# Kernel tuning notes

Hardware: AMD Instinct MI355X
Metric: run time of the kernel (lower is better)

Reference implementation:

```python
import jax, jax.numpy as jnp
import numpy as np

NA, NPA, NT = 4096, 8192, 4096  # authors, papers, terms
HEADS = 8

def _ln(x, g, b):
    m = jnp.mean(x, -1, keepdims=True)
    v = jnp.var(x, -1, keepdims=True)
    return (x - m) * jax.lax.rsqrt(v + 1e-5) * g + b

def _gat(x_src, x_dst, src, dst, W, a_s, a_d, b, n_dst):
    # PyG-style GATConv (shared lin for src/dst, no self loops), per edge type.
    heads, outc = a_s.shape
    h_s = (x_src @ W).reshape(-1, heads, outc)
    h_d = (x_dst @ W).reshape(-1, heads, outc)
    e = jax.nn.leaky_relu(jnp.sum(h_s * a_s, -1)[src] + jnp.sum(h_d * a_d, -1)[dst], 0.2)  # [E,H]
    m = jax.ops.segment_max(e, dst, num_segments=n_dst)
    m = jnp.where(jnp.isfinite(m), m, 0.0)
    w = jnp.exp(e - m[dst])
    den = jax.ops.segment_sum(w, dst, num_segments=n_dst)
    alpha = w / (den[dst] + 1e-16)
    out = jax.ops.segment_sum(h_s[src] * alpha[..., None], dst, num_segments=n_dst)
    return out.reshape(n_dst, heads * outc) + b

def _gtl(x, peQ, peK, db, Wq, bq, Wk, bk, Wv, bv, Wo, bo, g1, be1, Wf1, bf1, Wf2, bf2, g2, be2):
    # PE-modulated dense multi-head attention + FFN, pre/post LN residual blocks.
    N, D = x.shape
    dh = D // HEADS
    Q = (x @ Wq + bq + peQ).reshape(N, HEADS, dh)
    K = (x @ Wk + bk + peK).reshape(N, HEADS, dh)
    V = (x @ Wv + bv).reshape(N, HEADS, dh)
    s = jnp.einsum('nhd,mhd->hnm', Q, K) / jnp.sqrt(jnp.float32(dh)) + db[None, None, :]
    o = jnp.einsum('hnm,mhd->nhd', jax.nn.softmax(s, -1), V).reshape(N, D) @ Wo + bo
    x = _ln(x + o, g1, be1)
    f = jax.nn.relu(x @ Wf1 + bf1) @ Wf2 + bf2
    return _ln(x + f, g2, be2)

def _forward(F, I):
    (x_author, x_paper, x_term, original_A, t1_W, t1_b, t2_W, t2_b, t3_W, t3_b,
     gat1_W, gat1_as, gat1_ad, gat1_b, gat2_W, gat2_as, gat2_ad, gat2_b,
     pe_embed, peWQ, peWK,
     gt_Wq, gt_bq, gt_Wk, gt_bk, gt_Wv, gt_bv, gt_Wo, gt_bo,
     gt_g1, gt_be1, gt_Wf1, gt_bf1, gt_Wf2, gt_bf2, gt_g2, gt_be2,
     cat_W, cat_b, mlp_W1, mlp_b1, mlp_W2, mlp_b2) = F
    (ap_src, ap_dst, pa_src, pa_dst, pt_src, pt_dst, tp_src, tp_dst, deg) = I
    xa = jax.nn.relu(x_author @ t1_W + t1_b)
    xp = jax.nn.relu(x_paper @ t2_W + t2_b)
    xt = jax.nn.relu(x_term @ t3_W + t3_b)
    # to_hetero GAT layer 1 (heads=8, out=128): sum over incoming edge types, relu
    h_p1 = jax.nn.relu(_gat(xa, xp, ap_src, ap_dst, gat1_W[0], gat1_as[0], gat1_ad[0], gat1_b[0], NPA)
                       + _gat(xt, xp, tp_src, tp_dst, gat1_W[3], gat1_as[3], gat1_ad[3], gat1_b[3], NPA))
    h_a1 = jax.nn.relu(_gat(xp, xa, pa_src, pa_dst, gat1_W[1], gat1_as[1], gat1_ad[1], gat1_b[1], NA))
    # layer 2 (heads=1); only author output feeds the graph transformer
    h_a2 = _gat(h_p1, h_a1, pa_src, pa_dst, gat2_W[1], gat2_as[1], gat2_ad[1], gat2_b[1], NA)
    # learned positional encodings + adjacency reconstruction loss
    peQ = pe_embed @ peWQ
    peK = pe_embed @ peWK
    S = jax.nn.sigmoid(peQ @ peK.T)  # [NA, NA]
    loss_pe = jnp.mean((S[None] - original_A) ** 2)
    db = jnp.log(jnp.maximum(deg.astype(jnp.float32), 1.0))  # degree key bias
    x = h_a2
    outs = [x]
    for i in range(gt_Wq.shape[0]):
        x = _gtl(x, peQ, peK, db, gt_Wq[i], gt_bq[i], gt_Wk[i], gt_bk[i], gt_Wv[i], gt_bv[i],
                 gt_Wo[i], gt_bo[i], gt_g1[i], gt_be1[i], gt_Wf1[i], gt_bf1[i], gt_Wf2[i], gt_bf2[i],
                 gt_g2[i], gt_be2[i])
        outs.append(x)
    x_gt = jax.nn.relu(jnp.concatenate(outs, -1) @ cat_W + cat_b)
    logits = jax.nn.relu(x_gt @ mlp_W1 + mlp_b1) @ mlp_W2 + mlp_b2
    return loss_pe, jax.nn.softmax(logits, -1), x_gt

def setup_inputs() -> dict:
    key = jax.random.key(0)
    ks = iter(jax.random.split(key, 100))
    def rn(sh, s=1.0):
        return jax.random.normal(next(ks), sh, jnp.float32) * s
    def ri(sh, hi, lo=0):
        return jax.random.randint(next(ks), sh, lo, hi)
    d = {}
    d['x_author'] = rn((NA, 334)); d['x_paper'] = rn((NPA, 512)); d['x_term'] = rn((NT, 128))
    d['ap_src'] = ri((80000,), NA); d['ap_dst'] = ri((80000,), NPA)
    d['pa_src'] = ri((80000,), NPA); d['pa_dst'] = ri((80000,), NA)
    d['pt_src'] = ri((160000,), NPA); d['pt_dst'] = ri((160000,), NT)
    d['tp_src'] = ri((160000,), NT); d['tp_dst'] = ri((160000,), NPA)
    d['original_A'] = (jax.random.uniform(next(ks), (4, NA, NA)) < 0.005).astype(jnp.float32)
    d['deg'] = ri((NA,), 64, 1)
    p = 0.05
    d['t1_W'] = rn((334, 128), p); d['t1_b'] = jnp.zeros((128,))
    d['t2_W'] = rn((512, 128), p); d['t2_b'] = jnp.zeros((128,))
    d['t3_W'] = rn((128, 128), p); d['t3_b'] = jnp.zeros((128,))
    d['gat1_W'] = rn((4, 128, 1024), p); d['gat1_as'] = rn((4, 8, 128), p)
    d['gat1_ad'] = rn((4, 8, 128), p); d['gat1_b'] = jnp.zeros((4, 1024))
    d['gat2_W'] = rn((4, 1024, 128), p); d['gat2_as'] = rn((4, 1, 128), p)
    d['gat2_ad'] = rn((4, 1, 128), p); d['gat2_b'] = jnp.zeros((4, 128))
    d['pe_embed'] = rn((NA, 128), p); d['peWQ'] = rn((128, 128), p); d['peWK'] = rn((128, 128), p)
    d['gt_Wq'] = rn((2, 128, 128), p); d['gt_bq'] = jnp.zeros((2, 128))
    d['gt_Wk'] = rn((2, 128, 128), p); d['gt_bk'] = jnp.zeros((2, 128))
    d['gt_Wv'] = rn((2, 128, 128), p); d['gt_bv'] = jnp.zeros((2, 128))
    d['gt_Wo'] = rn((2, 128, 128), p); d['gt_bo'] = jnp.zeros((2, 128))
    d['gt_g1'] = jnp.ones((2, 128)); d['gt_be1'] = jnp.zeros((2, 128))
    d['gt_Wf1'] = rn((2, 128, 256), p); d['gt_bf1'] = jnp.zeros((2, 256))
    d['gt_Wf2'] = rn((2, 256, 128), p); d['gt_bf2'] = jnp.zeros((2, 128))
    d['gt_g2'] = jnp.ones((2, 128)); d['gt_be2'] = jnp.zeros((2, 128))
    d['cat_W'] = rn((384, 128), p); d['cat_b'] = jnp.zeros((128,))
    d['mlp_W1'] = rn((128, 256), p); d['mlp_b1'] = jnp.zeros((256,))
    d['mlp_W2'] = rn((256, 4), p); d['mlp_b2'] = jnp.zeros((4,))
    return d

def reference(x_author, x_paper, x_term, ap_src, ap_dst, pa_src, pa_dst, pt_src, pt_dst, tp_src, tp_dst, original_A, deg, t1_W, t1_b, t2_W, t2_b, t3_W, t3_b, gat1_W, gat1_as, gat1_ad, gat1_b, gat2_W, gat2_as, gat2_ad, gat2_b, pe_embed, peWQ, peWK, gt_Wq, gt_bq, gt_Wk, gt_bk, gt_Wv, gt_bv, gt_Wo, gt_bo, gt_g1, gt_be1, gt_Wf1, gt_bf1, gt_Wf2, gt_bf2, gt_g2, gt_be2, cat_W, cat_b, mlp_W1, mlp_b1, mlp_W2, mlp_b2):
    F = (x_author, x_paper, x_term, original_A, t1_W, t1_b, t2_W, t2_b, t3_W, t3_b,
         gat1_W, gat1_as, gat1_ad, gat1_b, gat2_W, gat2_as, gat2_ad, gat2_b,
         pe_embed, peWQ, peWK,
         gt_Wq, gt_bq, gt_Wk, gt_bk, gt_Wv, gt_bv, gt_Wo, gt_bo,
         gt_g1, gt_be1, gt_Wf1, gt_bf1, gt_Wf2, gt_bf2, gt_g2, gt_be2,
         cat_W, cat_b, mlp_W1, mlp_b1, mlp_W2, mlp_b2)
    I = (ap_src, ap_dst, pa_src, pa_dst, pt_src, pt_dst, tp_src, tp_dst, deg)
    return _forward(F, I)
```

## Files before the change

kernel.cpp:

```cpp
#include <hip/hip_runtime.h>
#include <math.h>

#define NA   4096
#define NPA  8192
#define NT   4096
#define E_AP 80000
#define E_PA 80000
#define E_TP 160000
#define E_TOT (E_AP + E_TP + E_PA)
#define NSLOT (NPA + NPA + NA)
#define ASPLIT 4

typedef __attribute__((ext_vector_type(4))) float f32x4;
typedef __attribute__((ext_vector_type(8))) short s16x8;
typedef __attribute__((ext_vector_type(8))) unsigned short u16x8;
typedef unsigned short ushort_t;

__device__ __forceinline__ ushort_t f2bf(float f){
  unsigned u = __float_as_uint(f);
  unsigned r = u + 0x7fffu + ((u >> 16) & 1u);
  return (ushort_t)(r >> 16);
}
__device__ __forceinline__ float bf2f(ushort_t u){
  return __uint_as_float(((unsigned)u) << 16);
}

template<int ACT, int TN>
__global__ __launch_bounds__(256) void gemm_mfma_k(
    const void* __restrict__ Ain, const void* __restrict__ A2in, const void* __restrict__ A3in,
    int aBf16,
    const float* __restrict__ B, void* __restrict__ Cout, int cBf16,
    const float* __restrict__ bias,
    const float* __restrict__ addmat, int addCols, int addLd,
    const float* __restrict__ lng, const float* __restrict__ lnb,
    float* __restrict__ rdOut,
    int M, int N, int K, int lda, int ldb, int ldc)
{
  const char* A  = (const char*)Ain;
  const char* A2 = (const char*)A2in;
  const char* A3 = (const char*)A3in;
  char* C = (char*)Cout;

  __shared__ __align__(16) ushort_t As[64][40];
  __shared__ __align__(16) ushort_t Bs[TN][40];
  constexpr int NJ = TN / 32;
  int bm = blockIdx.x * 64, bn = blockIdx.y * TN;
  int tid = threadIdx.x;
  int w = tid >> 6, lane = tid & 63, lg = lane >> 4, lid = lane & 15;
  int wm = (w & 1) * 32, wn = (w >> 1) * (TN / 2);
  f32x4 acc[2][NJ];
#pragma unroll
  for (int i = 0; i < 2; ++i)
#pragma unroll
    for (int j = 0; j < NJ; ++j) acc[i][j] = (f32x4){0.f, 0.f, 0.f, 0.f};

  for (int k0 = 0; k0 < K; k0 += 32) {
    {
      int r = tid >> 2, ks = (tid & 3) * 8;
      int kcol = k0 + ks;
      const char* Ab = A;
      if (A2) { int seg = kcol >> 7; Ab = (seg == 0) ? A : ((seg == 1) ? A2 : A3); kcol &= 127; }
      u16x8 v;
      if (aBf16) {
        v = *(const u16x8*)((const ushort_t*)Ab + (size_t)(bm + r) * lda + kcol);
      } else {
        const float* ap = (const float*)Ab + (size_t)(bm + r) * lda + kcol;
#pragma unroll
        for (int j = 0; j < 8; ++j) {
          int gk = k0 + ks + j;
          float fv = (gk < K) ? ap[j] : 0.f;
          v[j] = f2bf(fv);
        }
      }
      *(u16x8*)&As[r][ks] = v;
    }
    if (TN == 128) {
      int n = tid >> 1, ks = (tid & 1) * 16;
      ushort_t tmp[16];
#pragma unroll
      for (int j = 0; j < 16; ++j) {
        int gk = k0 + ks + j;
        float fv = (gk < K) ? B[(size_t)gk * ldb + bn + n] : 0.f;
        tmp[j] = f2bf(fv);
      }
      u16x8 v0, v1;
#pragma unroll
      for (int j = 0; j < 8; ++j) { v0[j] = tmp[j]; v1[j] = tmp[8 + j]; }
      *(u16x8*)&Bs[n][ks] = v0;
      *(u16x8*)&Bs[n][ks + 8] = v1;
    } else {
      int n = tid >> 2, ks = (tid & 3) * 8;
      u16x8 v;
#pragma unroll
      for (int j = 0; j < 8; ++j) {
        int gk = k0 + ks + j;
        float fv = (gk < K) ? B[(size_t)gk * ldb + bn + n] : 0.f;
        v[j] = f2bf(fv);
      }
      *(u16x8*)&Bs[n][ks] = v;
    }
    __syncthreads();
    s16x8 a_frag[2], b_frag[NJ];
#pragma unroll
    for (int i = 0; i < 2; ++i) a_frag[i] = *(s16x8*)&As[wm + i * 16 + lid][lg * 8];
#pragma unroll
    for (int j = 0; j < NJ; ++j) b_frag[j] = *(s16x8*)&Bs[wn + j * 16 + lid][lg * 8];
#pragma unroll
    for (int i = 0; i < 2; ++i)
#pragma unroll
      for (int j = 0; j < NJ; ++j)
        acc[i][j] = __builtin_amdgcn_mfma_f32_16x16x32_bf16(a_frag[i], b_frag[j], acc[i][j], 0, 0, 0);
    __syncthreads();
  }
  if constexpr (ACT == 3) {
    __shared__ float Ct[64][132];
#pragma unroll
    for (int i = 0; i < 2; ++i) {
#pragma unroll
      for (int j = 0; j < NJ; ++j) {
        int coll = wn + j * 16 + lid;
#pragma unroll
        for (int rr = 0; rr < 4; ++rr) {
          int rowl = wm + i * 16 + lg * 4 + rr;
          Ct[rowl][coll] = acc[i][j][rr];
        }
      }
    }
    __syncthreads();
    int row = tid >> 2, part = tid & 3;
    const float* vsel = (bm + row < 8192) ? lng : lnb;
    float rd = 0.f;
    ushort_t* Cu = (ushort_t*)C;
#pragma unroll
    for (int c2 = 0; c2 < 32; ++c2) {
      int c = part * 32 + c2;
      float f = Ct[row][c];
      rd = fmaf(f, vsel[c], rd);
      Cu[(size_t)(bm + row) * ldc + c] = f2bf(f);
    }
    rd += __shfl_xor(rd, 1);
    rd += __shfl_xor(rd, 2);
    if (part == 0) rdOut[bm + row] = rd;
  } else {
#pragma unroll
    for (int i = 0; i < 2; ++i) {
#pragma unroll
      for (int j = 0; j < NJ; ++j) {
        int c = bn + wn + j * 16 + lid;
#pragma unroll
        for (int rr = 0; rr < 4; ++rr) {
          int r = bm + wm + i * 16 + lg * 4 + rr;
          float v = acc[i][j][rr];
          if (bias)   v += bias[c];
          if (addmat && c < addCols) v += addmat[(size_t)r * addLd + c];
          if (ACT == 1) v = fmaxf(v, 0.f);
          if (cBf16) ((ushort_t*)C)[(size_t)r * ldc + c] = f2bf(v);
          else       ((float*)C)[(size_t)r * ldc + c] = v;
        }
      }
    }
  }
}

struct GDesc {
  const void* A; const void* A2;
  const float* B; void* C;
  const float* bias;
  int aBf16, cBf16, act;
  int M, N, K, lda, ldb, ldc;
  int nz, aOffZ, bOffZ, cOffZ;
  int tileStart;
};
struct GDescArr { GDesc d[4]; int nd; };

__global__ __launch_bounds__(256) void gemm_multi_k(GDescArr da){
  int t = blockIdx.x;
  int di = 0;
#pragma unroll
  for (int i = 1; i < 4; ++i) if (i < da.nd && t >= da.d[i].tileStart) di = i;
  const int aBf16 = da.d[di].aBf16, cBf16 = da.d[di].cBf16, act = da.d[di].act;
  const int M = da.d[di].M, N = da.d[di].N, K = da.d[di].K;
  const int lda = da.d[di].lda, ldb = da.d[di].ldb, ldc = da.d[di].ldc;
  int local = t - da.d[di].tileStart;
  int tM = M >> 6;
  int perZ = tM * (N >> 6);
  int z = local / perZ, rem = local - z * perZ;
  int bm = (rem % tM) * 64, bn = (rem / tM) * 64;
  int asz = aBf16 ? 2 : 4;
  const char* A  = (const char*)da.d[di].A  + (size_t)z * da.d[di].aOffZ * asz;
  const char* A2 = da.d[di].A2 ? (const char*)da.d[di].A2 + (size_t)z * da.d[di].aOffZ * asz : nullptr;
  const float* B = da.d[di].B + (size_t)z * da.d[di].bOffZ;
  char* C = (char*)da.d[di].C + (size_t)z * da.d[di].cOffZ * (cBf16 ? 2 : 4);
  const float* bias = da.d[di].bias ? da.d[di].bias + (size_t)z * da.d[di].cOffZ : nullptr;

  __shared__ __align__(16) ushort_t As[64][40];
  __shared__ __align__(16) ushort_t Bs[64][40];
  int tid = threadIdx.x;
  int w = tid >> 6, lane = tid & 63, lg = lane >> 4, lid = lane & 15;
  int wm = (w & 1) * 32, wn = (w >> 1) * 32;
  f32x4 acc[2][2];
#pragma unroll
  for (int i = 0; i < 2; ++i)
#pragma unroll
    for (int j = 0; j < 2; ++j) acc[i][j] = (f32x4){0.f, 0.f, 0.f, 0.f};

  for (int k0 = 0; k0 < K; k0 += 32) {
    {
      int r = tid >> 2, ks = (tid & 3) * 8;
      int kcol = k0 + ks;
      const char* Ab = A;
      if (A2) { int seg = kcol >> 7; Ab = seg ? A2 : A; kcol &= 127; }
      u16x8 v;
      if (aBf16) {
        v = *(const u16x8*)((const ushort_t*)Ab + (size_t)(bm + r) * lda + kcol);
      } else {
        const float* ap = (const float*)Ab + (size_t)(bm + r) * lda + kcol;
#pragma unroll
        for (int j = 0; j < 8; ++j) {
          int gk = k0 + ks + j;
          float fv = (gk < K) ? ap[j] : 0.f;
          v[j] = f2bf(fv);
        }
      }
      *(u16x8*)&As[r][ks] = v;
    }
    {
      int n = tid >> 2, ks = (tid & 3) * 8;
      u16x8 v;
#pragma unroll
      for (int j = 0; j < 8; ++j) {
        int gk = k0 + ks + j;
        float fv = (gk < K) ? B[(size_t)gk * ldb + bn + n] : 0.f;
        v[j] = f2bf(fv);
      }
      *(u16x8*)&Bs[n][ks] = v;
    }
    __syncthreads();
    s16x8 a_frag[2], b_frag[2];
#pragma unroll
    for (int i = 0; i < 2; ++i) a_frag[i] = *(s16x8*)&As[wm + i * 16 + lid][lg * 8];
#pragma unroll
    for (int j = 0; j < 2; ++j) b_frag[j] = *(s16x8*)&Bs[wn + j * 16 + lid][lg * 8];
#pragma unroll
    for (int i = 0; i < 2; ++i)
#pragma unroll
      for (int j = 0; j < 2; ++j)
        acc[i][j] = __builtin_amdgcn_mfma_f32_16x16x32_bf16(a_frag[i], b_frag[j], acc[i][j], 0, 0, 0);
    __syncthreads();
  }
#pragma unroll
  for (int i = 0; i < 2; ++i) {
#pragma unroll
    for (int j = 0; j < 2; ++j) {
      int c = bn + wn + j * 16 + lid;
#pragma unroll
      for (int rr = 0; rr < 4; ++rr) {
        int r = bm + wm + i * 16 + lg * 4 + rr;
        float v = acc[i][j][rr];
        if (bias) v += bias[c];
        if (act == 1) v = fmaxf(v, 0.f);
        if (cBf16) ((ushort_t*)C)[(size_t)r * ldc + c] = f2bf(v);
        else       ((float*)C)[(size_t)r * ldc + c] = v;
      }
    }
  }
}

__global__ void prep_k(const float* __restrict__ gat1_b, const float* __restrict__ gat1_W,
                       const float* __restrict__ Wq, const float* __restrict__ bq,
                       const float* __restrict__ Wk, const float* __restrict__ bk,
                       const float* __restrict__ Wv, const float* __restrict__ bv,
                       const float* __restrict__ peWQ, const float* __restrict__ peWK,
                       const int* __restrict__ deg,
                       const float* __restrict__ gat1_as, const float* __restrict__ gat1_ad,
                       const int* __restrict__ ap_dst, const int* __restrict__ tp_dst,
                       const int* __restrict__ pa_dst,
                       const float* __restrict__ gt_Wo, const float* __restrict__ gt_Wf1,
                       const float* __restrict__ gt_Wf2, const float* __restrict__ cat_W,
                       const float* __restrict__ mlp_W1,
                       float* __restrict__ bsum, float* __restrict__ Wqkv,
                       float* __restrict__ bqkv, float* __restrict__ peW,
                       float* __restrict__ Bstack, float* __restrict__ dbv,
                       float* __restrict__ Ps, float* __restrict__ Pd,
                       int* __restrict__ cnt,
                       ushort_t* __restrict__ Wot, ushort_t* __restrict__ Wf1t,
                       ushort_t* __restrict__ Wf2t, ushort_t* __restrict__ catt,
                       ushort_t* __restrict__ mlp1t, ushort_t* __restrict__ Wqkvt)
{
  int idx = blockIdx.x * blockDim.x + threadIdx.x;
  if (idx < 1024) { bsum[idx] = gat1_b[idx] + gat1_b[3 * 1024 + idx]; return; }
  idx -= 1024;
  if (idx < 2 * 128 * 384) {
    int l = idx / 49152, rem = idx % 49152;
    int k = rem / 384, c = rem % 384;
    float v;
    if (c < 128)      v = Wq[(size_t)l * 16384 + k * 128 + c];
    else if (c < 256) v = Wk[(size_t)l * 16384 + k * 128 + c - 128];
    else              v = Wv[(size_t)l * 16384 + k * 128 + c - 256];
    Wqkv[(size_t)l * 49152 + k * 384 + c] = v;
    return;
  }
  idx -= 2 * 128 * 384;
  if (idx < 2 * 384) {
    int l = idx / 384, c = idx % 384;
    float v;
    if (c < 128)      v = bq[l * 128 + c];
    else if (c < 256) v = bk[l * 128 + c - 128];
    else              v = bv[l * 128 + c - 256];
    bqkv[l * 384 + c] = v;
    return;
  }
  idx -= 2 * 384;
  if (idx < 128 * 256) {
    int k = idx / 256, c = idx % 256;
    peW[k * 256 + c] = (c < 128) ? peWQ[k * 128 + c] : peWK[k * 128 + c - 128];
    return;
  }
  idx -= 128 * 256;
  if (idx < 256 * 1024) {
    int k = idx / 1024, c = idx % 1024;
    Bstack[idx] = (k < 128) ? gat1_W[(size_t)k * 1024 + c]
                            : gat1_W[(size_t)3 * 131072 + (size_t)(k - 128) * 1024 + c];
    return;
  }
  idx -= 256 * 1024;
  if (idx < NA) { dbv[idx] = logf(fmaxf((float)deg[idx], 1.f)); return; }
  idx -= NA;
  if (idx < 3 * 1024) {
    const int wsel[3] = {0, 3, 1};
    int type = idx / 1024, rem = idx % 1024;
    int k = rem >> 3, h = rem & 7;
    const float* wr = gat1_W + (size_t)wsel[type] * 131072 + (size_t)k * 1024 + h * 128;
    const float* a1 = gat1_as + wsel[type] * 1024 + h * 128;
    const float* a2 = gat1_ad + wsel[type] * 1024 + h * 128;
    float s1 = 0.f, s2 = 0.f;
    for (int c = 0; c < 128; ++c){ float wv = wr[c]; s1 = fmaf(wv, a1[c], s1); s2 = fmaf(wv, a2[c], s2); }
    Ps[(size_t)type * 1024 + k * 8 + h] = s1;
    Pd[(size_t)type * 1024 + k * 8 + h] = s2;
    return;
  }
  idx -= 3 * 1024;
  if (idx < E_TOT) {
    int slot;
    if (idx < E_AP)             slot = ap_dst[idx];
    else if (idx < E_AP + E_TP) slot = NPA + tp_dst[idx - E_AP];
    else                        slot = 2 * NPA + pa_dst[idx - E_AP - E_TP];
    atomicAdd(&cnt[slot], 1);
    return;
  }
  idx -= E_TOT;
  if (idx < 2 * 128 * 128) {
    int l = idx / 16384, rem = idx % 16384;
    int n = rem / 128, k = rem % 128;
    Wot[idx] = f2bf(gt_Wo[(size_t)l * 16384 + k * 128 + n]);
    return;
  }
  idx -= 2 * 128 * 128;
  if (idx < 2 * 256 * 128) {
    int l = idx / 32768, rem = idx % 32768;
    int n = rem / 128, k = rem % 128;
    Wf1t[idx] = f2bf(gt_Wf1[(size_t)l * 32768 + k * 256 + n]);
    return;
  }
  idx -= 2 * 256 * 128;
  if (idx < 2 * 128 * 256) {
    int l = idx / 32768, rem = idx % 32768;
    int n = rem / 256, k = rem % 256;
    Wf2t[idx] = f2bf(gt_Wf2[(size_t)l * 32768 + k * 128 + n]);
    return;
  }
  idx -= 2 * 128 * 256;
  if (idx < 128 * 384) {
    int n = idx / 384, k = idx % 384;
    catt[idx] = f2bf(cat_W[(size_t)k * 128 + n]);
    return;
  }
  idx -= 128 * 384;
  if (idx < 256 * 128) {
    int n = idx / 128, k = idx % 128;
    mlp1t[idx] = f2bf(mlp_W1[(size_t)k * 256 + n]);
    return;
  }
  idx -= 256 * 128;
  if (idx < 2 * 384 * 128) {
    int l = idx / 49152, rem = idx % 49152;
    int n = rem / 128, k = rem % 128;
    float v;
    if (n < 128)      v = Wq[(size_t)l * 16384 + k * 128 + n];
    else if (n < 256) v = Wk[(size_t)l * 16384 + k * 128 + n - 128];
    else              v = Wv[(size_t)l * 16384 + k * 128 + n - 256];
    Wqkvt[idx] = f2bf(v);
  }
}

__global__ void scatterf_k(const int* __restrict__ ap_dst, const int* __restrict__ tp_dst,
                           const int* __restrict__ pa_dst, const int* __restrict__ off,
                           int* __restrict__ cur, int* __restrict__ eidx){
  int i = blockIdx.x * blockDim.x + threadIdx.x;
  if (i >= E_TOT) return;
  int slot, local;
  if (i < E_AP)             { local = i;                 slot = ap_dst[local]; }
  else if (i < E_AP + E_TP) { local = i - E_AP;          slot = NPA + tp_dst[local]; }
  else                      { local = i - E_AP - E_TP;   slot = 2 * NPA + pa_dst[local]; }
  int p = atomicAdd(&cur[slot], 1);
  eidx[off[slot] + p] = local;
}

__global__ __launch_bounds__(1024) void exscan_k(const int* __restrict__ in, int* __restrict__ out, int n){
  __shared__ int wsum[16];
  __shared__ int carrySh;
  int t = threadIdx.x, w = t >> 6, lane = t & 63;
  if (t == 0) carrySh = 0;
  __syncthreads();
  for (int base = 0; base < n; base += 1024){
    int carry = carrySh;
    int v = (base + t < n) ? in[base + t] : 0;
    int sc = v;
#pragma unroll
    for (int o2 = 1; o2 < 64; o2 <<= 1){
      int u = __shfl_up(sc, o2);
      if (lane >= o2) sc += u;
    }
    if (lane == 63) wsum[w] = sc;
    __syncthreads();
    int wadd = 0;
#pragma unroll
    for (int i = 0; i < 15; ++i) if (i < w) wadd += wsum[i];
    if (base + t < n) out[base + t] = carry + wadd + sc - v;
    if (t == 1023) carrySh = carry + wadd + sc;
    __syncthreads();
  }
}

__global__ __launch_bounds__(256) void scorev_k(
    const ushort_t* __restrict__ xa, const ushort_t* __restrict__ xp, const ushort_t* __restrict__ xt,
    const float* __restrict__ Ps, const float* __restrict__ Pd, float* __restrict__ scores)
{
  int r = blockIdx.x * 4 + (threadIdx.x >> 6);
  int lane = threadIdx.x & 63;
  const ushort_t* x; const float* P; int row;
  if (r < 4096)       { x = xa; P = Ps;        row = r; }
  else if (r < 12288) { x = xp; P = Pd;        row = r - 4096; }
  else if (r < 16384) { x = xt; P = Ps + 1024; row = r - 12288; }
  else if (r < 24576) { x = xp; P = Pd + 1024; row = r - 16384; }
  else if (r < 32768) { x = xp; P = Ps + 2048; row = r - 24576; }
  else                { x = xa; P = Pd + 2048; row = r - 32768; }
  unsigned u = *(const unsigned*)(x + (size_t)row * 128 + 2 * lane);
  float x0 = bf2f((ushort_t)(u & 0xffff));
  float x1 = bf2f((ushort_t)(u >> 16));
  float res[8];
#pragma unroll
  for (int h = 0; h < 8; ++h) {
    float s = x0 * P[(2 * lane) * 8 + h] + x1 * P[(2 * lane + 1) * 8 + h];
#pragma unroll
    for (int o = 32; o; o >>= 1) s += __shfl_down(s, o);
    res[h] = s;
  }
  if (lane == 0) {
#pragma unroll
    for (int h = 0; h < 8; ++h) scores[(size_t)r * 8 + h] = res[h];
  }
}

__global__ __launch_bounds__(256) void agg8ff_k(
    const int* __restrict__ eidx, const int* __restrict__ off, const int* __restrict__ cnt,
    const int* __restrict__ ap_src, const int* __restrict__ tp_src, const int* __restrict__ pa_src,
    const ushort_t* __restrict__ xa, const ushort_t* __restrict__ xt, const ushort_t* __restrict__ xp,
    const float* __restrict__ scores, ushort_t* __restrict__ agg)
{
  int g = blockIdx.x * 4 + (threadIdx.x >> 6);
  if (g >= NSLOT) return;
  const int* src; const ushort_t* x; const float* ssb; const float* sdb; int d;
  if (g < NPA)          { src = ap_src; x = xa; ssb = scores;                     sdb = scores + (size_t)4096 * 8;  d = g; }
  else if (g < 2 * NPA) { src = tp_src; x = xt; ssb = scores + (size_t)12288 * 8; sdb = scores + (size_t)16384 * 8; d = g - NPA; }
  else                  { src = pa_src; x = xp; ssb = scores + (size_t)24576 * 8; sdb = scores + (size_t)32768 * 8; d = g - 2 * NPA; }
  int lane = threadIdx.x & 63;
  int hh = lane & 7;
  float sdv = sdb[(size_t)d * 8 + hh];
  int base = off[g], n = cnt[g];
  float mh = -1e30f, den = 0.f;
  float acc0[8], acc1[8];
#pragma unroll
  for (int h2 = 0; h2 < 8; ++h2){ acc0[h2] = 0.f; acc1[h2] = 0.f; }
  int e = (n > 0) ? eidx[base] : 0;
  int s = (n > 0) ? src[e] : 0;
  for (int k = 0; k < n; ++k){
    int en = 0, sn = 0;
    if (k + 1 < n){ en = eidx[base + k + 1]; sn = src[en]; }
    float v = ssb[(size_t)s * 8 + hh] + sdv;
    v = v > 0.f ? v : 0.2f * v;
    float mn = fmaxf(mh, v);
    float sc = __expf(mh - mn);
    float wv_ = __expf(v - mn);
    den = den * sc + wv_;
    mh = mn;
    unsigned u = *(const unsigned*)(x + (size_t)s * 128 + 2 * lane);
    float xv0 = bf2f((ushort_t)(u & 0xffff));
    float xv1 = bf2f((ushort_t)(u >> 16));
#pragma unroll
    for (int h2 = 0; h2 < 8; ++h2){
      float sch = __shfl(sc, h2);
      float wh = __shfl(wv_, h2);
      acc0[h2] = fmaf(wh, xv0, acc0[h2] * sch);
      acc1[h2] = fmaf(wh, xv1, acc1[h2] * sch);
    }
    e = en; s = sn;
  }
  ushort_t* o = agg + (size_t)g * 1024;
#pragma unroll
  for (int h2 = 0; h2 < 8; ++h2){
    float dh = __shfl(den, h2) + 1e-16f;
    unsigned pk = (unsigned)f2bf(acc0[h2] / dh) | ((unsigned)f2bf(acc1[h2] / dh) << 16);
    *(unsigned*)(o + h2 * 128 + 2 * lane) = pk;
  }
}

__global__ __launch_bounds__(256) void gat_agg1f_k(
    const int* __restrict__ eidx, const int* __restrict__ off, const int* __restrict__ cnt,
    const int* __restrict__ src, const ushort_t* __restrict__ hs,
    const float* __restrict__ sArr,
    const float* __restrict__ bias, float* __restrict__ outp, int Ndst)
{
  int d = blockIdx.x * 4 + (threadIdx.x >> 6);
  if (d >= Ndst) return;
  int lane = threadIdx.x & 63;
  float sdv = sArr[8192 + d];
  int base = off[d], n = cnt[d];
  float mh = -1e30f, den = 0.f, a0 = 0.f, a1 = 0.f;
  int e = (n > 0) ? eidx[base] : 0;
  int s = (n > 0) ? src[e] : 0;
  for (int k = 0; k < n; ++k){
    int en = 0, sn = 0;
    if (k + 1 < n){ en = eidx[base + k + 1]; sn = src[en]; }
    float v = sArr[s] + sdv;
    v = v > 0.f ? v : 0.2f * v;
    float mn = fmaxf(mh, v);
    float sc = __expf(mh - mn);
    float w_ = __expf(v - mn);
    den = den * sc + w_;
    mh = mn;
    unsigned u = *(const unsigned*)(hs + (size_t)s * 128 + 2 * lane);
    a0 = fmaf(w_, bf2f((ushort_t)(u & 0xffff)), a0 * sc);
    a1 = fmaf(w_, bf2f((ushort_t)(u >> 16)), a1 * sc);
    e = en; s = sn;
  }
  float inv = 1.f / (den + 1e-16f);
  outp[(size_t)d * 128 + 2 * lane]     = a0 * inv + bias[2 * lane];
  outp[(size_t)d * 128 + 2 * lane + 1] = a1 * inv + bias[2 * lane + 1];
}

__global__ __launch_bounds__(256) void loss_mfma_k(const float* __restrict__ peQ,
    const float* __restrict__ peK, const float* __restrict__ A4, float* __restrict__ lossAcc)
{
  __shared__ __align__(16) ushort_t As[64][40];
  __shared__ __align__(16) ushort_t Bs[128][40];
  __shared__ float sig[64][128];
  __shared__ float red[256];
  int br = blockIdx.x * 64, bc = blockIdx.y * 128;
  int tid = threadIdx.x;
  int w = tid >> 6, lane = tid & 63, lg = lane >> 4, lid = lane & 15;
  int wm = (w & 1) * 32, wn = (w >> 1) * 64;
  f32x4 acc[2][4];
#pragma unroll
  for (int i = 0; i < 2; ++i)
#pragma unroll
    for (int j = 0; j < 4; ++j) acc[i][j] = (f32x4){0.f, 0.f, 0.f, 0.f};

  for (int k0 = 0; k0 < 128; k0 += 32) {
    {
      int r = tid >> 2, ks = (tid & 3) * 8;
      const float* ap = peQ + (size_t)(br + r) * 256 + k0 + ks;
      u16x8 v;
#pragma unroll
      for (int j = 0; j < 8; ++j) v[j] = f2bf(ap[j]);
      *(u16x8*)&As[r][ks] = v;
    }
    {
      int n = tid >> 1, ks = (tid & 1) * 16;
      const float* bp = peK + (size_t)(bc + n) * 256 + k0 + ks;
      u16x8 v0, v1;
#pragma unroll
      for (int j = 0; j < 8; ++j) { v0[j] = f2bf(bp[j]); v1[j] = f2bf(bp[8 + j]); }
      *(u16x8*)&Bs[n][ks] = v0;
      *(u16x8*)&Bs[n][ks + 8] = v1;
    }
    __syncthreads();
    s16x8 a_frag[2], b_frag[4];
#pragma unroll
    for (int i = 0; i < 2; ++i) a_frag[i] = *(s16x8*)&As[wm + i * 16 + lid][lg * 8];
#pragma unroll
    for (int j = 0; j < 4; ++j) b_frag[j] = *(s16x8*)&Bs[wn + j * 16 + lid][lg * 8];
#pragma unroll
    for (int i = 0; i < 2; ++i)
#pragma unroll
      for (int j = 0; j < 4; ++j)
        acc[i][j] = __builtin_amdgcn_mfma_f32_16x16x32_bf16(a_frag[i], b_frag[j], acc[i][j], 0, 0, 0);
    __syncthreads();
  }
#pragma unroll
  for (int i = 0; i < 2; ++i) {
#pragma unroll
    for (int rr = 0; rr < 4; ++rr) {
      int row = wm + i * 16 + lg * 4 + rr;
#pragma unroll
      for (int j = 0; j < 4; ++j) {
        int col = wn + j * 16 + lid;
        sig[row][col] = 1.f / (1.f + __expf(-acc[i][j][rr]));
      }
    }
  }
  __syncthreads();
  float err = 0.f;
#pragma unroll
  for (int it = 0; it < 8; ++it) {
    int idx = tid + it * 256;
    int rr = idx >> 5, c4 = idx & 31;
    float4 s4 = *(const float4*)&sig[rr][c4 * 4];
    size_t o = (size_t)(br + rr) * 4096 + bc + c4 * 4;
#pragma unroll
    for (int q = 0; q < 4; ++q) {
      float4 a = *(const float4*)&A4[(size_t)q * 16777216 + o];
      float d0 = s4.x - a.x, d1 = s4.y - a.y, d2 = s4.z - a.z, d3 = s4.w - a.w;
      err += d0 * d0 + d1 * d1 + d2 * d2 + d3 * d3;
    }
  }
  red[tid] = err;
  __syncthreads();
  for (int o = 128; o; o >>= 1){
    if (tid < o) red[tid] += red[tid + o];
    __syncthreads();
  }
  if (tid == 0) atomicAdd(lossAcc, red[0]);
}

__global__ __launch_bounds__(256) void attn_mfma_k(
    const ushort_t* __restrict__ Q, const ushort_t* __restrict__ K, const ushort_t* __restrict__ V,
    const float* __restrict__ dbv, float* __restrict__ part)
{
  const int ld = 384;
  int h = blockIdx.y, sp = blockIdx.z;
  int qbase = blockIdx.x * 64;
  int tid = threadIdx.x;
  int w = tid >> 6, lane = tid & 63, lid = lane & 15, lg = lane >> 4;
  __shared__ __align__(16) ushort_t Vt[16][72];
  __shared__ __align__(16) ushort_t Pl[4][16][72];
  __shared__ float dbs[64];

  s16x8 qf;
  if (lg < 2) {
    u16x8 v = *(const u16x8*)(Q + (size_t)(qbase + 16 * w + lid) * ld + h * 16 + 8 * lg);
#pragma unroll
    for (int j = 0; j < 8; ++j) v[j] = f2bf(bf2f(v[j]) * 0.25f);
    qf = (s16x8)v;
  } else {
    qf = (s16x8){0,0,0,0,0,0,0,0};
  }

  float m = -1e30f, l = 0.f;
  f32x4 o = {0.f, 0.f, 0.f, 0.f};

  int kb0 = sp * (4096 / ASPLIT);
  for (int kt = 0; kt < 4096 / ASPLIT; kt += 64) {
    int kb = kb0 + kt;
    __syncthreads();
    {
      int key = tid >> 2, ds_ = (tid & 3) * 4;
      const ushort_t* vp = V + (size_t)(kb + key) * ld + h * 16 + ds_;
#pragma unroll
      for (int j = 0; j < 4; ++j) Vt[ds_ + j][key] = vp[j];
      if (tid < 64) dbs[tid] = dbv[kb + tid];
    }
    __syncthreads();

    f32x4 s[4];
#pragma unroll
    for (int g = 0; g < 4; ++g) {
      s16x8 kf;
      if (lg < 2) {
        kf = (s16x8)(*(const u16x8*)(K + (size_t)(kb + 16 * g + lid) * ld + h * 16 + 8 * lg));
      } else kf = (s16x8){0,0,0,0,0,0,0,0};
      s[g] = __builtin_amdgcn_mfma_f32_16x16x32_bf16(kf, qf, (f32x4){0.f,0.f,0.f,0.f}, 0, 0, 0);
    }
#pragma unroll
    for (int g = 0; g < 4; ++g)
#pragma unroll
      for (int r = 0; r < 4; ++r) s[g][r] += dbs[16 * g + 4 * lg + r];

    float tmax = -1e30f;
#pragma unroll
    for (int g = 0; g < 4; ++g)
#pragma unroll
      for (int r = 0; r < 4; ++r) tmax = fmaxf(tmax, s[g][r]);
    tmax = fmaxf(tmax, __shfl_xor(tmax, 16));
    tmax = fmaxf(tmax, __shfl_xor(tmax, 32));
    float mn = fmaxf(m, tmax);
    float scale = __expf(m - mn);
    float psum = 0.f;
    float p[4][4];
#pragma unroll
    for (int g = 0; g < 4; ++g)
#pragma unroll
      for (int r = 0; r < 4; ++r) { p[g][r] = __expf(s[g][r] - mn); psum += p[g][r]; }
    psum += __shfl_xor(psum, 16);
    psum += __shfl_xor(psum, 32);
    l = l * scale + psum;
    m = mn;

#pragma unroll
    for (int g = 0; g < 4; ++g) {
#pragma unroll
      for (int rp = 0; rp < 4; rp += 2) {
        unsigned pack = (unsigned)f2bf(p[g][rp]) | ((unsigned)f2bf(p[g][rp + 1]) << 16);
        *(unsigned*)&Pl[w][lid][16 * g + 4 * lg + rp] = pack;
      }
    }
// ... 360 lines not shown
  float* out = (float*)d_out;

  char* base = (char*)d_ws;
  size_t off = 0;
  auto alloc = [&](size_t nbytes) -> void* {
    void* p = base + off;
    off += (nbytes + 255) & ~(size_t)255;
    return p;
  };
  ushort_t* xa  = (ushort_t*)alloc((size_t)NA * 128 * 2);
  ushort_t* xp  = (ushort_t*)alloc((size_t)NPA * 128 * 2);
  ushort_t* xt  = (ushort_t*)alloc((size_t)NT * 128 * 2);
  ushort_t* accP = (ushort_t*)alloc((size_t)NPA * 1024 * 2);
  ushort_t* accA = (ushort_t*)alloc((size_t)NA * 1024 * 2);
  ushort_t* agg  = (ushort_t*)alloc((size_t)NSLOT * 1024 * 2);
  float* scores = (float*)alloc((size_t)36864 * 8 * 4);
  float* Ps   = (float*)alloc(3 * 1024 * 4);
  float* Pd   = (float*)alloc(3 * 1024 * 4);
  ushort_t* hs2 = (ushort_t*)alloc((size_t)NPA * 128 * 2);
  ushort_t* hd2 = (ushort_t*)alloc((size_t)NA * 128 * 2);
  float* s2sd = (float*)alloc((size_t)(NPA + NA) * 4);
  float* hA2  = (float*)alloc((size_t)NA * 128 * 4);
  float* peQK = (float*)alloc((size_t)NA * 256 * 4);
  float* dbv  = (float*)alloc((size_t)NA * 4);
  float* bsum = (float*)alloc(1024 * 4);
  float* Wqkv = (float*)alloc((size_t)2 * 128 * 384 * 4);
  float* bqkv = (float*)alloc((size_t)2 * 384 * 4);
  float* peW  = (float*)alloc((size_t)128 * 256 * 4);
  float* Bstack = (float*)alloc((size_t)256 * 1024 * 4);
  ushort_t* Wot   = (ushort_t*)alloc((size_t)2 * 128 * 128 * 2);
  ushort_t* Wf1t  = (ushort_t*)alloc((size_t)2 * 256 * 128 * 2);
  ushort_t* Wf2t  = (ushort_t*)alloc((size_t)2 * 128 * 256 * 2);
  ushort_t* catt  = (ushort_t*)alloc((size_t)128 * 384 * 2);
  ushort_t* mlp1t = (ushort_t*)alloc((size_t)256 * 128 * 2);
  ushort_t* Wqkvt = (ushort_t*)alloc((size_t)2 * 384 * 128 * 2);
  ushort_t* QKVb = (ushort_t*)alloc((size_t)NA * 384 * 2);
  float* outs1= (float*)alloc((size_t)NA * 128 * 4);
  int*   offb = (int*)alloc((size_t)NSLOT * 4);
  int*   eidx = (int*)alloc((size_t)E_TOT * 4);
  size_t zstart = off;
  int*      cnt   = (int*)alloc((size_t)NSLOT * 4);
  int*      cur   = (int*)alloc((size_t)NSLOT * 4);
  float*    lossAcc = (float*)alloc(256);
  size_t zlen = off - zstart;

  float* part = (float*)accP;

  if (off > ws_size){
    setval_k<<<1, 1, 0, stream>>>(out, -12345.0f);
    return;
  }

  auto gemmx = [&](int act, int tn, const void* A, const void* A2, const void* A3, int aBf16,
                   const float* B, void* C, int cBf16, const float* bias,
                   const float* addmat, int addCols, int addLd,
                   const float* lng, const float* lnb, float* rdOut,
                   int M, int N, int K, int lda, int ldb, int ldc){
    dim3 g(M / 64, N / tn, 1);
    if (tn == 128) {
      if (act == 0)      gemm_mfma_k<0,128><<<g, 256, 0, stream>>>(A, A2, A3, aBf16, B, C, cBf16, bias, addmat, addCols, addLd, lng, lnb, rdOut, M, N, K, lda, ldb, ldc);
      else if (act == 1) gemm_mfma_k<1,128><<<g, 256, 0, stream>>>(A, A2, A3, aBf16, B, C, cBf16, bias, addmat, addCols, addLd, lng, lnb, rdOut, M, N, K, lda, ldb, ldc);
      else               gemm_mfma_k<3,128><<<g, 256, 0, stream>>>(A, A2, A3, aBf16, B, C, cBf16, bias, addmat, addCols, addLd, lng, lnb, rdOut, M, N, K, lda, ldb, ldc);
    } else {
      if (act == 0)      gemm_mfma_k<0,64><<<g, 256, 0, stream>>>(A, A2, A3, aBf16, B, C, cBf16, bias, addmat, addCols, addLd, lng, lnb, rdOut, M, N, K, lda, ldb, ldc);
      else               gemm_mfma_k<1,64><<<g, 256, 0, stream>>>(A, A2, A3, aBf16, B, C, cBf16, bias, addmat, addCols, addLd, lng, lnb, rdOut, M, N, K, lda, ldb, ldc);
    }
  };

  hipMemsetAsync(base + zstart, 0, zlen, stream);
  prep_k<<<4165, 256, 0, stream>>>(gat1_b, gat1_W, gt_Wq, gt_bq, gt_Wk, gt_bk, gt_Wv, gt_bv,
                                   peWQ, peWK, deg, gat1_as, gat1_ad, ap_dst, tp_dst, pa_dst,
                                   gt_Wo, gt_Wf1, gt_Wf2, cat_W, mlp_W1,
                                   bsum, Wqkv, bqkv, peW, Bstack, dbv, Ps, Pd, cnt,
                                   Wot, Wf1t, Wf2t, catt, mlp1t, Wqkvt);
  {
    GDescArr da; da.nd = 4;
    da.d[0] = { x_author, nullptr, t1_W, xa, t1_b, 0, 1, 1, NA, 128, 334, 334, 128, 128, 1, 0, 0, 0, 0 };
    da.d[1] = { x_paper,  nullptr, t2_W, xp, t2_b, 0, 1, 1, NPA, 128, 512, 512, 128, 128, 1, 0, 0, 0, 128 };
    da.d[2] = { x_term,   nullptr, t3_W, xt, t3_b, 0, 1, 1, NT, 128, 128, 128, 128, 128, 1, 0, 0, 0, 384 };
    da.d[3] = { pe_embed, nullptr, peW, peQK, nullptr, 0, 0, 0, NA, 256, 128, 128, 256, 256, 1, 0, 0, 0, 512 };
    gemm_multi_k<<<768, 256, 0, stream>>>(da);
  }
  exscan_k<<<1, 1024, 0, stream>>>(cnt, offb, NSLOT);
  scatterf_k<<<(E_TOT + 255) / 256, 256, 0, stream>>>(ap_dst, tp_dst, pa_dst, offb, cur, eidx);
  scorev_k<<<9216, 256, 0, stream>>>(xa, xp, xt, Ps, Pd, scores);
  agg8ff_k<<<NSLOT / 4, 256, 0, stream>>>(eidx, offb, cnt, ap_src, tp_src, pa_src,
                                          xa, xt, xp, scores, agg);
  {
    GDescArr da; da.nd = 2;
    da.d[0] = { agg, agg + (size_t)NPA * 1024, Bstack, accP, bsum, 1, 1, 1,
                NPA, 128, 256, 1024, 1024, 1024, 8, 128, 128, 128, 0 };
    da.d[1] = { agg + (size_t)2 * NPA * 1024, nullptr, gat1_W + 131072, accA, gat1_b + 1024, 1, 1, 1,
                NA, 128, 128, 1024, 1024, 1024, 8, 128, 128, 128, 2048 };
    gemm_multi_k<<<3072, 256, 0, stream>>>(da);
  }
  gemmx(3, 128, accP, 0, 0, 1, gat2_W + 131072, hs2, 1, 0, 0, 0, 0,
        gat2_as + 128, gat2_ad + 128, s2sd, NPA + NA, 128, 1024, 1024, 128, 128);
  gat_agg1f_k<<<NA / 4, 256, 0, stream>>>(eidx, offb + 2 * NPA, cnt + 2 * NPA, pa_src, hs2, s2sd,
                                          gat2_b + 128, hA2, NA);
  loss_mfma_k<<<dim3(64, 32), 256, 0, stream>>>(peQK, peQK + 128, original_A, lossAcc);
  gemmx(0, 64, hA2, 0, 0, 0, Wqkv, QKVb, 1, bqkv, peQK, 256, 256,
        0, 0, 0, NA, 384, 128, 128, 384, 384);
  attn_mfma_k<<<dim3(NA / 64, 8, ASPLIT), 256, 0, stream>>>(QKVb, QKVb + 128, QKVb + 256, dbv, part);
  gt_tail_k<0><<<NA / 16, 256, 0, stream>>>(part, Wot, gt_bo, hA2,
                                            gt_g1, gt_be1, Wf1t, gt_bf1, Wf2t, gt_bf2,
                                            gt_g2, gt_be2, outs1,
                                            Wqkvt + (size_t)49152, bqkv + 384, peQK, QKVb,
                                            nullptr, nullptr, nullptr, nullptr,
                                            nullptr, nullptr, nullptr, nullptr, nullptr, nullptr);
  attn_mfma_k<<<dim3(NA / 64, 8, ASPLIT), 256, 0, stream>>>(QKVb, QKVb + 128, QKVb + 256, dbv, part);
  gt_tail_k<1><<<NA / 16, 256, 0, stream>>>(part, Wot + 16384, gt_bo + 128, outs1,
                                            gt_g1 + 128, gt_be1 + 128, Wf1t + 32768, gt_bf1 + 256,
                                            Wf2t + 32768, gt_bf2 + 128,
                                            gt_g2 + 128, gt_be2 + 128, nullptr,
                                            nullptr, nullptr, nullptr, nullptr,
                                            hA2, outs1, catt, cat_b, mlp1t, mlp_b1,
                                            mlp_W2, mlp_b2, lossAcc, out);
}
```

Baseline: 638.9 us.

## Horizontally fuse loss with GAT GEMM and scatter with score kernels

Merges the loss MFMA kernel into the GAT-1 projection GEMM launch by dispatching on block index, and merges the edge scatter into the per-node score kernel. Independent work then shares one launch and can overlap: the memory-bound loss pass runs alongside the compute-bound GEMM tiles. The cost is that every block in the fused GEMM launch reserves 48KB of shared memory, which can lower occupancy for the GEMM tiles. Each launch also carries a block-index branch.

New measurement: 642.3 us. Within noise of the previous version (+0.5%).

```diff
diff --git a/kernel.cpp b/kernel.cpp
--- a/kernel.cpp
+++ b/kernel.cpp
@@ -7,9 +7,13 @@
 #define E_AP 80000
 #define E_PA 80000
 #define E_TP 160000
+#define E_TOT (E_AP + E_TP + E_TP/2)
+#undef E_TOT
 #define E_TOT (E_AP + E_TP + E_PA)
 #define NSLOT (NPA + NPA + NA)
 #define ASPLIT 4
+#define SCV_BLOCKS 9216
+#define SCT_BLOCKS ((E_TOT + 255) / 256)
 
 typedef __attribute__((ext_vector_type(4))) float f32x4;
 typedef __attribute__((ext_vector_type(8))) short s16x8;
@@ -173,8 +177,7 @@
 };
 struct GDescArr { GDesc d[4]; int nd; };
 
-__global__ __launch_bounds__(256) void gemm_multi_k(GDescArr da){
-  int t = blockIdx.x;
+__device__ __forceinline__ void multi_gemm_body(const GDescArr& da, int t, char* smem){
   int di = 0;
 #pragma unroll
   for (int i = 1; i < 4; ++i) if (i < da.nd && t >= da.d[i].tileStart) di = i;
@@ -193,8 +196,8 @@
   char* C = (char*)da.d[di].C + (size_t)z * da.d[di].cOffZ * (cBf16 ? 2 : 4);
   const float* bias = da.d[di].bias ? da.d[di].bias + (size_t)z * da.d[di].cOffZ : nullptr;
 
-  __shared__ __align__(16) ushort_t As[64][40];
-  __shared__ __align__(16) ushort_t Bs[64][40];
+  ushort_t (*As)[40] = (ushort_t(*)[40])smem;
+  ushort_t (*Bs)[40] = (ushort_t(*)[40])(smem + 5120);
   int tid = threadIdx.x;
   int w = tid >> 6, lane = tid & 63, lg = lane >> 4, lid = lane & 15;
   int wm = (w & 1) * 32, wn = (w >> 1) * 32;
@@ -264,6 +267,105 @@
       }
     }
   }
+}
+
+__global__ __launch_bounds__(256) void gemm_multi_k(GDescArr da){
+  __shared__ __align__(16) char smem[10240];
+  multi_gemm_body(da, blockIdx.x, smem);
+}
+
+__device__ __forceinline__ void loss_body(int lb, char* smem,
+    const float* __restrict__ peQ, const float* __restrict__ peK,
+    const float* __restrict__ A4, float* __restrict__ lossAcc)
+{
+  ushort_t (*As)[40] = (ushort_t(*)[40])smem;
+  ushort_t (*Bs)[40] = (ushort_t(*)[40])(smem + 5120);
+  float (*sig)[128]  = (float(*)[128])(smem + 15360);
+  float* red         = (float*)(smem + 48128);
+  int br = (lb & 63) * 64, bc = (lb >> 6) * 128;
+  int tid = threadIdx.x;
+  int w = tid >> 6, lane = tid & 63, lg = lane >> 4, lid = lane & 15;
+  int wm = (w & 1) * 32, wn = (w >> 1) * 64;
+  f32x4 acc[2][4];
+#pragma unroll
+  for (int i = 0; i < 2; ++i)
+#pragma unroll
+    for (int j = 0; j < 4; ++j) acc[i][j] = (f32x4){0.f, 0.f, 0.f, 0.f};
+
+  for (int k0 = 0; k0 < 128; k0 += 32) {
+    {
+      int r = tid >> 2, ks = (tid & 3) * 8;
+      const float* ap = peQ + (size_t)(br + r) * 256 + k0 + ks;
+      u16x8 v;
+#pragma unroll
+      for (int j = 0; j < 8; ++j) v[j] = f2bf(ap[j]);
+      *(u16x8*)&As[r][ks] = v;
+    }
+    {
+      int n = tid >> 1, ks = (tid & 1) * 16;
+      const float* bp = peK + (size_t)(bc + n) * 256 + k0 + ks;
+      u16x8 v0, v1;
+#pragma unroll
+      for (int j = 0; j < 8; ++j) { v0[j] = f2bf(bp[j]); v1[j] = f2bf(bp[8 + j]); }
+      *(u16x8*)&Bs[n][ks] = v0;
+      *(u16x8*)&Bs[n][ks + 8] = v1;
+    }
+    __syncthreads();
+    s16x8 a_frag[2], b_frag[4];
+#pragma unroll
+    for (int i = 0; i < 2; ++i) a_frag[i] = *(s16x8*)&As[wm + i * 16 + lid][lg * 8];
+#pragma unroll
+    for (int j = 0; j < 4; ++j) b_frag[j] = *(s16x8*)&Bs[wn + j * 16 + lid][lg * 8];
+#pragma unroll
+    for (int i = 0; i < 2; ++i)
+#pragma unroll
+      for (int j = 0; j < 4; ++j)
+        acc[i][j] = __builtin_amdgcn_mfma_f32_16x16x32_bf16(a_frag[i], b_frag[j], acc[i][j], 0, 0, 0);
+    __syncthreads();
+  }
+#pragma unroll
+  for (int i = 0; i < 2; ++i) {
+#pragma unroll
+    for (int rr = 0; rr < 4; ++rr) {
+      int row = wm + i * 16 + lg * 4 + rr;
+#pragma unroll
+      for (int j = 0; j < 4; ++j) {
+        int col = wn + j * 16 + lid;
+        sig[row][col] = 1.f / (1.f + __expf(-acc[i][j][rr]));
+      }
+    }
+  }
+  __syncthreads();
+  float err = 0.f;
+#pragma unroll
+  for (int it = 0; it < 8; ++it) {
+    int idx = tid + it * 256;
+    int rr = idx >> 5, c4 = idx & 31;
+    float4 s4 = *(const float4*)&sig[rr][c4 * 4];
+    size_t o = (size_t)(br + rr) * 4096 + bc + c4 * 4;
+#pragma unroll
+    for (int q = 0; q < 4; ++q) {
+      float4 a = *(const float4*)&A4[(size_t)q * 16777216 + o];
+      float d0 = s4.x - a.x, d1 = s4.y - a.y, d2 = s4.z - a.z, d3 = s4.w - a.w;
+      err += d0 * d0 + d1 * d1 + d2 * d2 + d3 * d3;
+    }
+  }
+  red[tid] = err;
+  __syncthreads();
+  for (int o = 128; o; o >>= 1){
+    if (tid < o) red[tid] += red[tid + o];
+    __syncthreads();
+  }
+  if (tid == 0) atomicAdd(lossAcc, red[0]);
+}
+
+__global__ __launch_bounds__(256) void d2loss_k(GDescArr da, int gemmTiles,
+    const float* __restrict__ peQ, const float* __restrict__ peK,
+    const float* __restrict__ A4, float* __restrict__ lossAcc)
+{
+  __shared__ __align__(16) char smem[49152];
+  if ((int)blockIdx.x < gemmTiles) multi_gemm_body(da, blockIdx.x, smem);
+  else loss_body(blockIdx.x - gemmTiles, smem, peQ, peK, A4, lossAcc);
 }
 
 __global__ void prep_k(const float* __restrict__ gat1_b, const float* __restrict__ gat1_W,
@@ -393,19 +495,6 @@
   }
 }
 
-__global__ void scatterf_k(const int* __restrict__ ap_dst, const int* __restrict__ tp_dst,
-                           const int* __restrict__ pa_dst, const int* __restrict__ off,
-                           int* __restrict__ cur, int* __restrict__ eidx){
-  int i = blockIdx.x * blockDim.x + threadIdx.x;
-  if (i >= E_TOT) return;
-  int slot, local;
-  if (i < E_AP)             { local = i;                 slot = ap_dst[local]; }
-  else if (i < E_AP + E_TP) { local = i - E_AP;          slot = NPA + tp_dst[local]; }
-  else                      { local = i - E_AP - E_TP;   slot = 2 * NPA + pa_dst[local]; }
-  int p = atomicAdd(&cur[slot], 1);
-  eidx[off[slot] + p] = local;
-}
-
 __global__ __launch_bounds__(1024) void exscan_k(const int* __restrict__ in, int* __restrict__ out, int n){
   __shared__ int wsum[16];
   __shared__ int carrySh;
@@ -432,33 +521,46 @@
   }
 }
 
-__global__ __launch_bounds__(256) void scorev_k(
+__global__ __launch_bounds__(256) void score_scatter_k(
     const ushort_t* __restrict__ xa, const ushort_t* __restrict__ xp, const ushort_t* __restrict__ xt,
-    const float* __restrict__ Ps, const float* __restrict__ Pd, float* __restrict__ scores)
+    const float* __restrict__ Ps, const float* __restrict__ Pd, float* __restrict__ scores,
+    const int* __restrict__ ap_dst, const int* __restrict__ tp_dst, const int* __restrict__ pa_dst,
+    const int* __restrict__ off, int* __restrict__ cur, int* __restrict__ eidx)
 {
-  int r = blockIdx.x * 4 + (threadIdx.x >> 6);
-  int lane = threadIdx.x & 63;
-  const ushort_t* x; const float* P; int row;
-  if (r < 4096)       { x = xa; P = Ps;        row = r; }
-  else if (r < 12288) { x = xp; P = Pd;        row = r - 4096; }
-  else if (r < 16384) { x = xt; P = Ps + 1024; row = r - 12288; }
-  else if (r < 24576) { x = xp; P = Pd + 1024; row = r - 16384; }
-  else if (r < 32768) { x = xp; P = Ps + 2048; row = r - 24576; }
-  else                { x = xa; P = Pd + 2048; row = r - 32768; }
-  unsigned u = *(const unsigned*)(x + (size_t)row * 128 + 2 * lane);
-  float x0 = bf2f((ushort_t)(u & 0xffff));
-  float x1 = bf2f((ushort_t)(u >> 16));
-  float res[8];
-#pragma unroll
-  for (int h = 0; h < 8; ++h) {
-    float s = x0 * P[(2 * lane) * 8 + h] + x1 * P[(2 * lane + 1) * 8 + h];
-#pragma unroll
-    for (int o = 32; o; o >>= 1) s += __shfl_down(s, o);
-    res[h] = s;
-  }
-  if (lane == 0) {
-#pragma unroll
-    for (int h = 0; h < 8; ++h) scores[(size_t)r * 8 + h] = res[h];
+  if ((int)blockIdx.x < SCV_BLOCKS) {
+    int r = blockIdx.x * 4 + (threadIdx.x >> 6);
+    int lane = threadIdx.x & 63;
+    const ushort_t* x; const float* P; int row;
+    if (r < 4096)       { x = xa; P = Ps;        row = r; }
+    else if (r < 12288) { x = xp; P = Pd;        row = r - 4096; }
+    else if (r < 16384) { x = xt; P = Ps + 1024; row = r - 12288; }
+    else if (r < 24576) { x = xp; P = Pd + 1024; row = r - 16384; }
+    else if (r < 32768) { x = xp; P = Ps + 2048; row = r - 24576; }
+    else                { x = xa; P = Pd + 2048; row = r - 32768; }
+    unsigned u = *(const unsigned*)(x + (size_t)row * 128 + 2 * lane);
+    float x0 = bf2f((ushort_t)(u & 0xffff));
+    float x1 = bf2f((ushort_t)(u >> 16));
+    float res[8];
+#pragma unroll
+    for (int h = 0; h < 8; ++h) {
+      float s = x0 * P[(2 * lane) * 8 + h] + x1 * P[(2 * lane + 1) * 8 + h];
+#pragma unroll
+      for (int o = 32; o; o >>= 1) s += __shfl_down(s, o);
+      res[h] = s;
+    }
+    if (lane == 0) {
+#pragma unroll
+      for (int h = 0; h < 8; ++h) scores[(size_t)r * 8 + h] = res[h];
+    }
+  } else {
+    int i = (blockIdx.x - SCV_BLOCKS) * 256 + threadIdx.x;
+    if (i >= E_TOT) return;
+    int slot, local;
+    if (i < E_AP)             { local = i;                 slot = ap_dst[local]; }
+    else if (i < E_AP + E_TP) { local = i - E_AP;          slot = NPA + tp_dst[local]; }
+    else                      { local = i - E_AP - E_TP;   slot = 2 * NPA + pa_dst[local]; }
+    int p = atomicAdd(&cur[slot], 1);
+    eidx[off[slot] + p] = local;
   }
 }
 
@@ -547,90 +649,6 @@
   float inv = 1.f / (den + 1e-16f);
   outp[(size_t)d * 128 + 2 * lane]     = a0 * inv + bias[2 * lane];
   outp[(size_t)d * 128 + 2 * lane + 1] = a1 * inv + bias[2 * lane + 1];
-}
-
-__global__ __launch_bounds__(256) void loss_mfma_k(const float* __restrict__ peQ,
-    const float* __restrict__ peK, const float* __restrict__ A4, float* __restrict__ lossAcc)
-{
-  __shared__ __align__(16) ushort_t As[64][40];
-  __shared__ __align__(16) ushort_t Bs[128][40];
-  __shared__ float sig[64][128];
-  __shared__ float red[256];
-  int br = blockIdx.x * 64, bc = blockIdx.y * 128;
-  int tid = threadIdx.x;
-  int w = tid >> 6, lane = tid & 63, lg = lane >> 4, lid = lane & 15;
-  int wm = (w & 1) * 32, wn = (w >> 1) * 64;
-  f32x4 acc[2][4];
-#pragma unroll
-  for (int i = 0; i < 2; ++i)
-#pragma unroll
-    for (int j = 0; j < 4; ++j) acc[i][j] = (f32x4){0.f, 0.f, 0.f, 0.f};
-
-  for (int k0 = 0; k0 < 128; k0 += 32) {
-    {
-      int r = tid >> 2, ks = (tid & 3) * 8;
-      const float* ap = peQ + (size_t)(br + r) * 256 + k0 + ks;
-      u16x8 v;
-#pragma unroll
-      for (int j = 0; j < 8; ++j) v[j] = f2bf(ap[j]);
-      *(u16x8*)&As[r][ks] = v;
-    }
-    {
-      int n = tid >> 1, ks = (tid & 1) * 16;
-      const float* bp = peK + (size_t)(bc + n) * 256 + k0 + ks;
-      u16x8 v0, v1;
-#pragma unroll
-      for (int j = 0; j < 8; ++j) { v0[j] = f2bf(bp[j]); v1[j] = f2bf(bp[8 + j]); }
-      *(u16x8*)&Bs[n][ks] = v0;
-      *(u16x8*)&Bs[n][ks + 8] = v1;
-    }
-    __syncthreads();
-    s16x8 a_frag[2], b_frag[4];
-#pragma unroll
-    for (int i = 0; i < 2; ++i) a_frag[i] = *(s16x8*)&As[wm + i * 16 + lid][lg * 8];
-#pragma unroll
-    for (int j = 0; j < 4; ++j) b_frag[j] = *(s16x8*)&Bs[wn + j * 16 + lid][lg * 8];
-#pragma unroll
-    for (int i = 0; i < 2; ++i)
-#pragma unroll
-      for (int j = 0; j < 4; ++j)
-        acc[i][j] = __builtin_amdgcn_mfma_f32_16x16x32_bf16(a_frag[i], b_frag[j], acc[i][j], 0, 0, 0);
-    __syncthreads();
-  }
-#pragma unroll
-  for (int i = 0; i < 2; ++i) {
-#pragma unroll
-    for (int rr = 0; rr < 4; ++rr) {
-      int row = wm + i * 16 + lg * 4 + rr;
-#pragma unroll
-      for (int j = 0; j < 4; ++j) {
-        int col = wn + j * 16 + lid;
-        sig[row][col] = 1.f / (1.f + __expf(-acc[i][j][rr]));
-      }
-    }
-  }
-  __syncthreads();
-  float err = 0.f;
-#pragma unroll
-  for (int it = 0; it < 8; ++it) {
-    int idx = tid + it * 256;
-    int rr = idx >> 5, c4 = idx & 31;
-    float4 s4 = *(const float4*)&sig[rr][c4 * 4];
-    size_t o = (size_t)(br + rr) * 4096 + bc + c4 * 4;
-#pragma unroll
-    for (int q = 0; q < 4; ++q) {
-      float4 a = *(const float4*)&A4[(size_t)q * 16777216 + o];
-      float d0 = s4.x - a.x, d1 = s4.y - a.y, d2 = s4.z - a.z, d3 = s4.w - a.w;
-      err += d0 * d0 + d1 * d1 + d2 * d2 + d3 * d3;
-    }
-  }
-  red[tid] = err;
-  __syncthreads();
-  for (int o = 128; o; o >>= 1){
-    if (tid < o) red[tid] += red[tid + o];
-    __syncthreads();
-  }
-  if (tid == 0) atomicAdd(lossAcc, red[0]);
 }
 
 __global__ __launch_bounds__(256) void attn_mfma_k(
@@ -1157,8 +1175,9 @@
     gemm_multi_k<<<768, 256, 0, stream>>>(da);
   }
   exscan_k<<<1, 1024, 0, stream>>>(cnt, offb, NSLOT);
-  scatterf_k<<<(E_TOT + 255) / 256, 256, 0, stream>>>(ap_dst, tp_dst, pa_dst, offb, cur, eidx);
-  scorev_k<<<9216, 256, 0, stream>>>(xa, xp, xt, Ps, Pd, scores);
+  score_scatter_k<<<SCV_BLOCKS + SCT_BLOCKS, 256, 0, stream>>>(xa, xp, xt, Ps, Pd, scores,
+                                                               ap_dst, tp_dst, pa_dst,
+                                                               offb, cur, eidx);
   agg8ff_k<<<NSLOT / 4, 256, 0, stream>>>(eidx, offb, cnt, ap_src, tp_src, pa_src,
                                           xa, xt, xp, scores, agg);
   {
@@ -1167,13 +1186,12 @@
                 NPA, 128, 256, 1024, 1024, 1024, 8, 128, 128, 128, 0 };
     da.d[1] = { agg + (size_t)2 * NPA * 1024, nullptr, gat1_W + 131072, accA, gat1_b + 1024, 1, 1, 1,
                 NA, 128, 128, 1024, 1024, 1024, 8, 128, 128, 128, 2048 };
-    gemm_multi_k<<<3072, 256, 0, stream>>>(da);
+    d2loss_k<<<3072 + 2048, 256, 0, stream>>>(da, 3072, peQK, peQK + 128, original_A, lossAcc);
   }
   gemmx(3, 128, accP, 0, 0, 1, gat2_W + 131072, hs2, 1, 0, 0, 0, 0,
         gat2_as + 128, gat2_ad + 128, s2sd, NPA + NA, 128, 1024, 1024, 128, 128);
   gat_agg1f_k<<<NA / 4, 256, 0, stream>>>(eidx, offb + 2 * NPA, cnt + 2 * NPA, pa_src, hs2, s2sd,
                                           gat2_b + 128, hA2, NA);
-  loss_mfma_k<<<dim3(64, 32), 256, 0, stream>>>(peQK, peQK + 128, original_A, lossAcc);
   gemmx(0, 64, hA2, 0, 0, 0, Wqkv, QKVb, 1, bqkv, peQK, 256, 256,
         0, 0, 0, NA, 384, 128, 128, 384, 384);
   attn_mfma_k<<<dim3(NA / 64, 8, ASPLIT), 256, 0, stream>>>(QKVb, QKVb + 128, QKVb + 256, dbv, part);
```
